# Performance work log

Measured on AMD Instinct MI355X. Metric: run time of the kernel, lower is better.

## Reference

```python
import jax, jax.numpy as jnp
import numpy as np

D_MODEL = 4096
D_FF = 11008

def _dequant_matmul(x, w_int, s):
    # x: [N, in], w_int: [out, in] int, s: [out, 1] -> [N, out]
    w = w_int.astype(jnp.float32) * s  # dequantized weight [out, in]
    return x @ w.T

def setup_inputs() -> dict:
    key = jax.random.key(0)
    ks = jax.random.split(key, 7)
    x = jax.random.normal(ks[0], (4, 2048, D_MODEL), dtype=jnp.float32)
    gate_w = jax.random.randint(ks[1], (D_FF, D_MODEL), -128, 128, dtype=jnp.int32)
    up_w = jax.random.randint(ks[2], (D_FF, D_MODEL), -128, 128, dtype=jnp.int32)
    down_w = jax.random.randint(ks[3], (D_MODEL, D_FF), -128, 128, dtype=jnp.int32)
    gate_s = jax.random.uniform(ks[4], (D_FF, 1), dtype=jnp.float32) * 0.01
    up_s = jax.random.uniform(ks[5], (D_FF, 1), dtype=jnp.float32) * 0.01
    down_s = jax.random.uniform(ks[6], (D_MODEL, 1), dtype=jnp.float32) * 0.01
    return {"x": x, "gate_w": gate_w, "gate_s": gate_s, "up_w": up_w,
            "up_s": up_s, "down_w": down_w, "down_s": down_s}

def reference(x, gate_w, gate_s, up_w, up_s, down_w, down_s):
    batch, seq_len, hidden = x.shape
    x_flat = x.reshape(-1, hidden).astype(jnp.float32)
    gate = _dequant_matmul(x_flat, gate_w, gate_s)
    up = _dequant_matmul(x_flat, up_w, up_s)
    h = jax.nn.silu(gate) * up
    out = _dequant_matmul(h, down_w, down_s)
    return out.astype(x.dtype).reshape(batch, seq_len, hidden)
```

## Files before the change

### kernel.cpp

```cpp
#include <hip/hip_runtime.h>


typedef __attribute__((ext_vector_type(8))) __bf16 bf16x8;
typedef __attribute__((ext_vector_type(4))) float f32x4;
typedef __attribute__((ext_vector_type(8))) unsigned short ushort8;
typedef __attribute__((ext_vector_type(4))) int i32x4;

#define D_MODEL 4096
#define D_FF    11008
#define NTOK    8192

static __device__ __forceinline__ unsigned short f32_to_bf16(float f) {
    union { float f; unsigned u; } v; v.f = f;
    unsigned r = v.u + 0x7fffu + ((v.u >> 16) & 1u);
    return (unsigned short)(r >> 16);
}
static __device__ __forceinline__ void gload_lds16(const void* g, void* l) {
    __builtin_amdgcn_global_load_lds(
        (const __attribute__((address_space(1))) void*)g,
        (__attribute__((address_space(3))) void*)l, 16, 0, 0);
}

__global__ __launch_bounds__(256)
void pack_gu_kernel(const int* __restrict__ gw, const int* __restrict__ uw,
                    signed char* __restrict__ out)
{
    long long i = ((long long)blockIdx.x * 256 + threadIdx.x) * 8;
    const int r = (int)(i >> 12);
    const int k = (int)(i & 4095);
    const int src_row = ((r >> 5) << 4) + (r & 15);
    const int* src = ((r >> 4) & 1) ? uw : gw;
    const int* p = src + (size_t)src_row * D_MODEL + k;
    int4 w0 = *(const int4*)(p);
    int4 w1 = *(const int4*)(p + 4);
    union { signed char c[8]; unsigned long long u; } rr;
    rr.c[0] = (signed char)w0.x; rr.c[1] = (signed char)w0.y;
    rr.c[2] = (signed char)w0.z; rr.c[3] = (signed char)w0.w;
    rr.c[4] = (signed char)w1.x; rr.c[5] = (signed char)w1.y;
    rr.c[6] = (signed char)w1.z; rr.c[7] = (signed char)w1.w;
    *(unsigned long long*)(out + i) = rr.u;
}

__global__ __launch_bounds__(256)
void dequant_w_kernel(const int* __restrict__ w, const float* __restrict__ s,
                      unsigned short* __restrict__ out, int cols, long long total)
{
    long long i = ((long long)blockIdx.x * 256 + threadIdx.x) * 8;
    if (i >= total) return;
    float sc = s[(int)(i / cols)];
    int4 w0 = *(const int4*)(w + i);
    int4 w1 = *(const int4*)(w + i + 4);
    ushort8 r;
    r[0] = f32_to_bf16((float)w0.x * sc);
    r[1] = f32_to_bf16((float)w0.y * sc);
    r[2] = f32_to_bf16((float)w0.z * sc);
    r[3] = f32_to_bf16((float)w0.w * sc);
    r[4] = f32_to_bf16((float)w1.x * sc);
    r[5] = f32_to_bf16((float)w1.y * sc);
    r[6] = f32_to_bf16((float)w1.z * sc);
    r[7] = f32_to_bf16((float)w1.w * sc);
    *(ushort8*)(out + i) = r;
}

__global__ __launch_bounds__(256)
void quant_x_kernel(const float* __restrict__ x, signed char* __restrict__ xq,
                    float* __restrict__ xs)
{
    __shared__ float red[4];
    const int row = blockIdx.x;
    const int t   = threadIdx.x;
    const float* xr = x + (size_t)row * D_MODEL;
    float4 v0 = *(const float4*)(xr + t * 16);
    float4 v1 = *(const float4*)(xr + t * 16 + 4);
    float4 v2 = *(const float4*)(xr + t * 16 + 8);
    float4 v3 = *(const float4*)(xr + t * 16 + 12);
    float m = fabsf(v0.x);
    m = fmaxf(m, fabsf(v0.y)); m = fmaxf(m, fabsf(v0.z)); m = fmaxf(m, fabsf(v0.w));
    m = fmaxf(m, fabsf(v1.x)); m = fmaxf(m, fabsf(v1.y)); m = fmaxf(m, fabsf(v1.z)); m = fmaxf(m, fabsf(v1.w));
    m = fmaxf(m, fabsf(v2.x)); m = fmaxf(m, fabsf(v2.y)); m = fmaxf(m, fabsf(v2.z)); m = fmaxf(m, fabsf(v2.w));
    m = fmaxf(m, fabsf(v3.x)); m = fmaxf(m, fabsf(v3.y)); m = fmaxf(m, fabsf(v3.z)); m = fmaxf(m, fabsf(v3.w));
    #pragma unroll
    for (int o = 32; o > 0; o >>= 1) m = fmaxf(m, __shfl_xor(m, o));
    if ((t & 63) == 0) red[t >> 6] = m;
    __syncthreads();
    m = fmaxf(fmaxf(red[0], red[1]), fmaxf(red[2], red[3]));
    m = fmaxf(m, 1e-20f);
    const float inv = 127.0f / m;
    if (t == 0) xs[row] = m / 127.0f;
    union { signed char c[16]; int4 i; } r;
    #pragma unroll
    for (int j = 0; j < 4; ++j) {
        float4 v = (j == 0) ? v0 : (j == 1) ? v1 : (j == 2) ? v2 : v3;
        r.c[j*4+0] = (signed char)(int)rintf(fminf(fmaxf(v.x*inv,-127.f),127.f));
        r.c[j*4+1] = (signed char)(int)rintf(fminf(fmaxf(v.y*inv,-127.f),127.f));
        r.c[j*4+2] = (signed char)(int)rintf(fminf(fmaxf(v.z*inv,-127.f),127.f));
        r.c[j*4+3] = (signed char)(int)rintf(fminf(fmaxf(v.w*inv,-127.f),127.f));
    }
    *(int4*)(xq + (size_t)row * D_MODEL + t * 16) = r.i;
}

__global__ __launch_bounds__(512, 2)
void gemm_i8gu(const signed char* __restrict__ A,
               const signed char* __restrict__ B,
               unsigned short* __restrict__ H,
               const float* __restrict__ xs,
               const float* __restrict__ gs,
               const float* __restrict__ us,
               int M, int NH, int K)
{
    extern __shared__ char smem[];
    const int tid = threadIdx.x;
    const int l   = tid & 63;
    const int w   = tid >> 6;
    const int wm  = w >> 2;
    const int wn  = w & 3;

    const int nbx  = gridDim.x;
    const int nwg  = nbx * gridDim.y;
    const int orig = blockIdx.y * nbx + blockIdx.x;
    const int cpx  = nwg >> 3;
    const int swz  = (orig & 7) * cpx + (orig >> 3);
    const int bn = swz % nbx, bm = swz / nbx;
    const int m0 = bm * 256, n0 = bn * 256;

    const int st_r = tid >> 2;
    const int st_c = ((tid & 3) ^ ((st_r >> 1) & 3)) << 4;
    const signed char* gA = A + (size_t)(m0 + st_r) * K + st_c;
    const signed char* gB = B + (size_t)(n0 + st_r) * K + st_c;
    const size_t ld128 = (size_t)128 * K;

    const int s4v = l >> 4;
    const int rA = wm * 128 + (l & 15);
    const int rB = wn * 64  + (l & 15);
    const int offA = rA * 64 + ((s4v << 4) ^ (((rA >> 1) & 3) << 4));
    const int offB = 16384 + rB * 64 + ((s4v << 4) ^ (((rB >> 1) & 3) << 4));

    i32x4 acc[8][4] = {};
    i32x4 af[8], bfr[4];

#define SBAR()  __builtin_amdgcn_sched_barrier(0)
#define BAR()   __builtin_amdgcn_s_barrier()
#define VM4()   asm volatile("s_waitcnt vmcnt(4)" ::: "memory")

#define ST_A8(SS, NXT) do { \
    const signed char* p_ = gA + ((size_t)(SS) << 6); \
    gload_lds16(p_,         smem + (NXT) + (w << 10)); \
    gload_lds16(p_ + ld128, smem + (NXT) + 8192 + (w << 10)); } while (0)
#define ST_B8(SS, NXT) do { \
    const signed char* p_ = gB + ((size_t)(SS) << 6); \
    gload_lds16(p_,         smem + (NXT) + 16384 + (w << 10)); \
    gload_lds16(p_ + 16384 - 8192 + 0, smem, 0); } while (0)
#undef ST_B8
#define ST_B8(SS, NXT) do { \
    const signed char* p_ = gB + ((size_t)(SS) << 6); \
    gload_lds16(p_,         smem + (NXT) + 16384 + (w << 10)); \
    gload_lds16(p_ + ld128, smem + (NXT) + 16384 + 8192 + (w << 10)); } while (0)

#define STEP8(CUR, NXT, SS) do { \
    ST_A8(SS, NXT); \
    ST_B8(SS, NXT); \
    af[0] = *(const i32x4*)(smem + (CUR) + offA); \
    af[1] = *(const i32x4*)(smem + (CUR) + offA + 1024); \
    af[2] = *(const i32x4*)(smem + (CUR) + offA + 2048); \
    af[3] = *(const i32x4*)(smem + (CUR) + offA + 3072); \
    af[4] = *(const i32x4*)(smem + (CUR) + offA + 4096); \
    af[5] = *(const i32x4*)(smem + (CUR) + offA + 5120); \
    af[6] = *(const i32x4*)(smem + (CUR) + offA + 6144); \
    af[7] = *(const i32x4*)(smem + (CUR) + offA + 7168); \
    bfr[0] = *(const i32x4*)(smem + (CUR) + offB); \
    bfr[1] = *(const i32x4*)(smem + (CUR) + offB + 1024); \
    bfr[2] = *(const i32x4*)(smem + (CUR) + offB + 2048); \
    bfr[3] = *(const i32x4*)(smem + (CUR) + offB + 3072); \
    __builtin_amdgcn_s_setprio(1); \
    _Pragma("unroll") \
    for (int mi_ = 0; mi_ < 8; ++mi_) { \
        _Pragma("unroll") \
        for (int ni_ = 0; ni_ < 4; ++ni_) { \
            acc[mi_][ni_] = __builtin_amdgcn_mfma_i32_16x16x64_i8( \
                af[mi_], bfr[ni_], acc[mi_][ni_], 0, 0, 0); \
        } } \
    __builtin_amdgcn_s_setprio(0); \
    VM4(); SBAR(); BAR(); \
} while (0)

    ST_A8(0, 0);      ST_B8(0, 0);
    ST_A8(1, 32768);  ST_B8(1, 32768);
    VM4(); SBAR(); BAR();

    const int T = K >> 6;
    #pragma unroll 1
    for (int s = 0; s < T; s += 4) {
        int s2 = s + 2; if (s2 >= T) s2 -= T;
        int s3 = s + 3; if (s3 >= T) s3 -= T;
        int s4 = s + 4; if (s4 >= T) s4 -= T;
        int s5 = s + 5; if (s5 >= T) s5 -= T;
        STEP8(0,     65536, s2);
        STEP8(32768, 98304, s3);
        STEP8(65536, 0,     s4);
        STEP8(98304, 32768, s5);
    }
    asm volatile("s_waitcnt vmcnt(0)" ::: "memory");

    const int er = (l >> 4) * 4;
    const int ec = l & 15;
    const int hbase = (n0 >> 1) + wn * 32;
    #pragma unroll
    for (int mi = 0; mi < 8; ++mi) {
        const int rowb = m0 + wm * 128 + mi * 16 + er;
        const float4 xsv = *(const float4*)(xs + rowb);
        #pragma unroll
        for (int p = 0; p < 2; ++p) {
            const int c = hbase + p * 16 + ec;
            const float sg = gs[c];
            const float su = us[c];
            #pragma unroll
            for (int q = 0; q < 4; ++q) {
                const float xsc = (q == 0) ? xsv.x : (q == 1) ? xsv.y
                                 : (q == 2) ? xsv.z : xsv.w;
                float g = (float)acc[mi][2*p][q]     * sg * xsc;
                float u = (float)acc[mi][2*p + 1][q] * su * xsc;
                float sig = 1.0f / (1.0f + __expf(-g));
                H[(size_t)(rowb + q) * NH + c] = f32_to_bf16(g * sig * u);
            }
        }
    }
#undef STEP8
#undef ST_A8
#undef ST_B8
#undef VM4
#undef BAR
#undef SBAR
}

__global__ __launch_bounds__(512, 2)
void gemm256_down(const unsigned short* __restrict__ A,
                  const unsigned short* __restrict__ B,
                  float* __restrict__ C,
                  int M, int N, int K)
{
    extern __shared__ char smem[];
    const int tid = threadIdx.x;
    const int l   = tid & 63;
    const int w   = tid >> 6;
    const int wm  = w >> 2;
    const int wn  = w & 3;

    const int nbx  = gridDim.x;
    const int nwg  = nbx * gridDim.y;
    const int orig = blockIdx.y * nbx + blockIdx.x;
    const int cpx  = nwg >> 3;
    const int swz  = (orig & 7) * cpx + (orig >> 3);
    const int bn = swz % nbx, bm = swz / nbx;
    const int m0 = bm * 256, n0 = bn * 256;

    const int st_r = tid >> 2;
    const int st_c = ((tid & 3) ^ ((st_r >> 1) & 3)) << 3;
    const unsigned short* gA = A + (size_t)(m0 + st_r) * K + st_c;
    const unsigned short* gB = B + (size_t)(n0 + st_r) * K + st_c;
    const size_t ld128 = (size_t)128 * K;

    const int s4v = l >> 4;
    const int rA = wm * 128 + (l & 15);
    const int rB = wn * 64  + (l & 15);
    const int offA = rA * 64 + ((s4v << 4) ^ (((rA >> 1) & 3) << 4));
    const int offB = 16384 + rB * 64 + ((s4v << 4) ^ (((rB >> 1) & 3) << 4));

    f32x4 acc[8][4] = {};
    bf16x8 af[8], bfr[4];

#define SBAR()  __builtin_amdgcn_sched_barrier(0)
#define BAR()   __builtin_amdgcn_s_barrier()
#define VM4()   asm volatile("s_waitcnt vmcnt(4)" ::: "memory")

#define ST_A2(SS, NXT) do { \
    const unsigned short* p_ = gA + ((size_t)(SS) << 5); \
    gload_lds16(p_,         smem + (NXT) + (w << 10)); \
    gload_lds16(p_ + ld128, smem + (NXT) + 8192 + (w << 10)); } while (0)
#define ST_B2(SS, NXT) do { \
    const unsigned short* p_ = gB + ((size_t)(SS) << 5); \
    gload_lds16(p_,         smem + (NXT) + 16384 + (w << 10)); \
    gload_lds16(p_ + ld128, smem + (NXT) + 16384 + 8192 + (w << 10)); } while (0)

#define STEPD(CUR, NXT, SS) do { \
    ST_A2(SS, NXT); \
    ST_B2(SS, NXT); \
    af[0] = *(const bf16x8*)(smem + (CUR) + offA); \
    af[1] = *(const bf16x8*)(smem + (CUR) + offA + 1024); \
    af[2] = *(const bf16x8*)(smem + (CUR) + offA + 2048); \
    af[3] = *(const bf16x8*)(smem + (CUR) + offA + 3072); \
    af[4] = *(const bf16x8*)(smem + (CUR) + offA + 4096); \
    af[5] = *(const bf16x8*)(smem + (CUR) + offA + 5120); \
    af[6] = *(const bf16x8*)(smem + (CUR) + offA + 6144); \
    af[7] = *(const bf16x8*)(smem + (CUR) + offA + 7168); \
    bfr[0] = *(const bf16x8*)(smem + (CUR) + offB); \
    bfr[1] = *(const bf16x8*)(smem + (CUR) + offB + 1024); \
    bfr[2] = *(const bf16x8*)(smem + (CUR) + offB + 2048); \
    bfr[3] = *(const bf16x8*)(smem + (CUR) + offB + 3072); \
    __builtin_amdgcn_s_setprio(1); \
    _Pragma("unroll") \
    for (int mi_ = 0; mi_ < 8; ++mi_) { \
        _Pragma("unroll") \
        for (int ni_ = 0; ni_ < 4; ++ni_) { \
            acc[mi_][ni_] = __builtin_amdgcn_mfma_f32_16x16x32_bf16( \
                af[mi_], bfr[ni_], acc[mi_][ni_], 0, 0, 0); \
        } } \
    __builtin_amdgcn_s_setprio(0); \
    VM4(); SBAR(); BAR(); \
} while (0)

    ST_A2(0, 0);      ST_B2(0, 0);
    ST_A2(1, 32768);  ST_B2(1, 32768);
    VM4(); SBAR(); BAR();

    const int T = K >> 5;
    #pragma unroll 1
    for (int s = 0; s < T; s += 4) {
        int s2 = s + 2; if (s2 >= T) s2 -= T;
        int s3 = s + 3; if (s3 >= T) s3 -= T;
        int s4 = s + 4; if (s4 >= T) s4 -= T;
        int s5 = s + 5; if (s5 >= T) s5 -= T;
        STEPD(0,     65536, s2);
        STEPD(32768, 98304, s3);
        STEPD(65536, 0,     s4);
        STEPD(98304, 32768, s5);
    }
    asm volatile("s_waitcnt vmcnt(0)" ::: "memory");

    const int er = (l >> 4) * 4;
    const int ec = l & 15;
    #pragma unroll
    for (int mi = 0; mi < 8; ++mi) {
        #pragma unroll
        for (int ni = 0; ni < 4; ++ni) {
            #pragma unroll
            for (int q = 0; q < 4; ++q) {
                int row = m0 + wm * 128 + mi * 16 + er + q;
                int col = n0 + wn * 64  + ni * 16 + ec;
                C[(size_t)row * N + col] = acc[mi][ni][q];
            }
        }
    }
#undef STEPD
#undef ST_A2
#undef ST_B2
#undef VM4
#undef BAR
#undef SBAR
}

extern "C" void kernel_launch(void* const* d_in, const int* in_sizes, int n_in,
                              void* d_out, int out_size, void* d_ws, size_t ws_size,
                              hipStream_t stream)
{
    const float* x  = (const float*)d_in[0];
    const int*   gw = (const int*)  d_in[1];
    const float* gs = (const float*)d_in[2];
    const int*   uw = (const int*)  d_in[3];
    const float* us = (const float*)d_in[4];
    const int*   dw = (const int*)  d_in[5];
    const float* dsc= (const float*)d_in[6];

    char* ws = (char*)d_ws;
    signed char*    Xq   = (signed char*)ws;    ws += (size_t)NTOK * D_MODEL;
    float*          xs   = (float*)ws;          ws += (size_t)NTOK * 4;
    signed char*    Wgu8 = (signed char*)ws;    ws += (size_t)2 * D_FF * D_MODEL;
    unsigned short* Wd   = (unsigned short*)ws; ws += (size_t)D_MODEL * D_FF * 2;
    unsigned short* H    = (unsigned short*)ws;

    const long long wtot  = (long long)D_FF * D_MODEL;
    const long long gutot = 2LL * wtot;

    hipFuncSetAttribute(reinterpret_cast<const void*>(gemm_i8gu),
                        hipFuncAttributeMaxDynamicSharedMemorySize, 131072);
    hipFuncSetAttribute(reinterpret_cast<const void*>(gemm256_down),
                        hipFuncAttributeMaxDynamicSharedMemorySize, 131072);

    pack_gu_kernel  <<<(int)(gutot / 2048), 256, 0, stream>>>(gw, uw, Wgu8);
    dequant_w_kernel<<<(int)(wtot  / 2048), 256, 0, stream>>>(dw, dsc, Wd, D_FF, wtot);
    quant_x_kernel  <<<NTOK, 256, 0, stream>>>(x, Xq, xs);

    dim3 g1(2 * D_FF / 256, NTOK / 256);
    gemm_i8gu<<<g1, 512, 131072, stream>>>(Xq, Wgu8, H, xs, gs, us,
                                           NTOK, D_FF, D_MODEL);

    dim3 g3(D_MODEL / 256, NTOK / 256);
    gemm256_down<<<g3, 512, 131072, stream>>>(H, Wd, (float*)d_out,
                                              NTOK, D_MODEL, D_FF);
}
```

Measured before the change: 1.555 ms.

## Deepen LDS prefetch to three stages and double-buffer B fragments in registers

Both GEMM kernels now issue global-to-LDS loads three K-steps ahead instead of two across the four-buffer LDS ring. They also load the next step's B fragments into a second register set while the current step's MFMAs run on the first. The aim is to hide more global-memory and LDS-read latency behind the matrix instructions. In exchange, each thread holds more live VGPRs, which risks pressure or spills under the 512-thread, 2-block launch bounds. The unchanged vmcnt(4) wait now forces two stages to land before each barrier, which may limit how much extra overlap is actually gained.

Result: no change. 1.563 ms (+0.5%).

```diff
diff --git a/kernel.cpp b/kernel.cpp
--- a/kernel.cpp
+++ b/kernel.cpp
@@ -136,7 +136,8 @@
     const int offB = 16384 + rB * 64 + ((s4v << 4) ^ (((rB >> 1) & 3) << 4));
 
     i32x4 acc[8][4] = {};
-    i32x4 af[8], bfr[4];
+    i32x4 af[8];
+    i32x4 bfa[4], bfb[4];
 
 #define SBAR()  __builtin_amdgcn_sched_barrier(0)
 #define BAR()   __builtin_amdgcn_s_barrier()
@@ -149,14 +150,15 @@
 #define ST_B8(SS, NXT) do { \
     const signed char* p_ = gB + ((size_t)(SS) << 6); \
     gload_lds16(p_,         smem + (NXT) + 16384 + (w << 10)); \
-    gload_lds16(p_ + 16384 - 8192 + 0, smem, 0); } while (0)
-#undef ST_B8
-#define ST_B8(SS, NXT) do { \
-    const signed char* p_ = gB + ((size_t)(SS) << 6); \
-    gload_lds16(p_,         smem + (NXT) + 16384 + (w << 10)); \
     gload_lds16(p_ + ld128, smem + (NXT) + 16384 + 8192 + (w << 10)); } while (0)
 
-#define STEP8(CUR, NXT, SS) do { \
+#define LD_BFR(BQ, BASE) do { \
+    BQ[0] = *(const i32x4*)(smem + (BASE) + offB); \
+    BQ[1] = *(const i32x4*)(smem + (BASE) + offB + 1024); \
+    BQ[2] = *(const i32x4*)(smem + (BASE) + offB + 2048); \
+    BQ[3] = *(const i32x4*)(smem + (BASE) + offB + 3072); } while (0)
+
+#define STEP8(CUR, RD, NXT, SS, BC, BN) do { \
     ST_A8(SS, NXT); \
     ST_B8(SS, NXT); \
     af[0] = *(const i32x4*)(smem + (CUR) + offA); \
@@ -167,17 +169,14 @@
     af[5] = *(const i32x4*)(smem + (CUR) + offA + 5120); \
     af[6] = *(const i32x4*)(smem + (CUR) + offA + 6144); \
     af[7] = *(const i32x4*)(smem + (CUR) + offA + 7168); \
-    bfr[0] = *(const i32x4*)(smem + (CUR) + offB); \
-    bfr[1] = *(const i32x4*)(smem + (CUR) + offB + 1024); \
-    bfr[2] = *(const i32x4*)(smem + (CUR) + offB + 2048); \
-    bfr[3] = *(const i32x4*)(smem + (CUR) + offB + 3072); \
+    LD_BFR(BN, RD); \
     __builtin_amdgcn_s_setprio(1); \
     _Pragma("unroll") \
     for (int mi_ = 0; mi_ < 8; ++mi_) { \
         _Pragma("unroll") \
         for (int ni_ = 0; ni_ < 4; ++ni_) { \
             acc[mi_][ni_] = __builtin_amdgcn_mfma_i32_16x16x64_i8( \
-                af[mi_], bfr[ni_], acc[mi_][ni_], 0, 0, 0); \
+                af[mi_], BC[ni_], acc[mi_][ni_], 0, 0, 0); \
         } } \
     __builtin_amdgcn_s_setprio(0); \
     VM4(); SBAR(); BAR(); \
@@ -185,19 +184,22 @@
 
     ST_A8(0, 0);      ST_B8(0, 0);
     ST_A8(1, 32768);  ST_B8(1, 32768);
-    VM4(); SBAR(); BAR();
+    ST_A8(2, 65536);  ST_B8(2, 65536);
+    VM4();
+    LD_BFR(bfa, 0);
+    SBAR(); BAR();
 
     const int T = K >> 6;
     #pragma unroll 1
     for (int s = 0; s < T; s += 4) {
-        int s2 = s + 2; if (s2 >= T) s2 -= T;
         int s3 = s + 3; if (s3 >= T) s3 -= T;
         int s4 = s + 4; if (s4 >= T) s4 -= T;
         int s5 = s + 5; if (s5 >= T) s5 -= T;
-        STEP8(0,     65536, s2);
-        STEP8(32768, 98304, s3);
-        STEP8(65536, 0,     s4);
-        STEP8(98304, 32768, s5);
+        int s6 = s + 6; if (s6 >= T) s6 -= T;
+        STEP8(0,     32768, 98304, s3, bfa, bfb);
+        STEP8(32768, 65536, 0,     s4, bfb, bfa);
+        STEP8(65536, 98304, 32768, s5, bfa, bfb);
+        STEP8(98304, 0,     65536, s6, bfb, bfa);
     }
     asm volatile("s_waitcnt vmcnt(0)" ::: "memory");
 
@@ -225,6 +227,7 @@
         }
     }
 #undef STEP8
+#undef LD_BFR
 #undef ST_A8
 #undef ST_B8
 #undef VM4
@@ -266,7 +269,8 @@
     const int offB = 16384 + rB * 64 + ((s4v << 4) ^ (((rB >> 1) & 3) << 4));
 
     f32x4 acc[8][4] = {};
-    bf16x8 af[8], bfr[4];
+    bf16x8 af[8];
+    bf16x8 bfa[4], bfb[4];
 
 #define SBAR()  __builtin_amdgcn_sched_barrier(0)
 #define BAR()   __builtin_amdgcn_s_barrier()
@@ -281,7 +285,13 @@
     gload_lds16(p_,         smem + (NXT) + 16384 + (w << 10)); \
     gload_lds16(p_ + ld128, smem + (NXT) + 16384 + 8192 + (w << 10)); } while (0)
 
-#define STEPD(CUR, NXT, SS) do { \
+#define LD_BFRD(BQ, BASE) do { \
+    BQ[0] = *(const bf16x8*)(smem + (BASE) + offB); \
+    BQ[1] = *(const bf16x8*)(smem + (BASE) + offB + 1024); \
+    BQ[2] = *(const bf16x8*)(smem + (BASE) + offB + 2048); \
+    BQ[3] = *(const bf16x8*)(smem + (BASE) + offB + 3072); } while (0)
+
+#define STEPD(CUR, RD, NXT, SS, BC, BN) do { \
     ST_A2(SS, NXT); \
     ST_B2(SS, NXT); \
     af[0] = *(const bf16x8*)(smem + (CUR) + offA); \
@@ -292,17 +302,14 @@
     af[5] = *(const bf16x8*)(smem + (CUR) + offA + 5120); \
     af[6] = *(const bf16x8*)(smem + (CUR) + offA + 6144); \
     af[7] = *(const bf16x8*)(smem + (CUR) + offA + 7168); \
-    bfr[0] = *(const bf16x8*)(smem + (CUR) + offB); \
-    bfr[1] = *(const bf16x8*)(smem + (CUR) + offB + 1024); \
-    bfr[2] = *(const bf16x8*)(smem + (CUR) + offB + 2048); \
-    bfr[3] = *(const bf16x8*)(smem + (CUR) + offB + 3072); \
+    LD_BFRD(BN, RD); \
     __builtin_amdgcn_s_setprio(1); \
     _Pragma("unroll") \
     for (int mi_ = 0; mi_ < 8; ++mi_) { \
         _Pragma("unroll") \
         for (int ni_ = 0; ni_ < 4; ++ni_) { \
             acc[mi_][ni_] = __builtin_amdgcn_mfma_f32_16x16x32_bf16( \
-                af[mi_], bfr[ni_], acc[mi_][ni_], 0, 0, 0); \
+                af[mi_], BC[ni_], acc[mi_][ni_], 0, 0, 0); \
         } } \
     __builtin_amdgcn_s_setprio(0); \
     VM4(); SBAR(); BAR(); \
@@ -310,19 +317,22 @@
 
     ST_A2(0, 0);      ST_B2(0, 0);
     ST_A2(1, 32768);  ST_B2(1, 32768);
-    VM4(); SBAR(); BAR();
+    ST_A2(2, 65536);  ST_B2(2, 65536);
+    VM4();
+    LD_BFRD(bfa, 0);
+    SBAR(); BAR();
 
     const int T = K >> 5;
     #pragma unroll 1
     for (int s = 0; s < T; s += 4) {
-        int s2 = s + 2; if (s2 >= T) s2 -= T;
         int s3 = s + 3; if (s3 >= T) s3 -= T;
         int s4 = s + 4; if (s4 >= T) s4 -= T;
         int s5 = s + 5; if (s5 >= T) s5 -= T;
-        STEPD(0,     65536, s2);
-        STEPD(32768, 98304, s3);
-        STEPD(65536, 0,     s4);
-        STEPD(98304, 32768, s5);
+        int s6 = s + 6; if (s6 >= T) s6 -= T;
+        STEPD(0,     32768, 98304, s3, bfa, bfb);
+        STEPD(32768, 65536, 0,     s4, bfb, bfa);
+        STEPD(65536, 98304, 32768, s5, bfa, bfb);
+        STEPD(98304, 0,     65536, s6, bfb, bfa);
     }
     asm volatile("s_waitcnt vmcnt(0)" ::: "memory");
 
@@ -341,6 +351,7 @@
         }
     }
 #undef STEPD
+#undef LD_BFRD
 #undef ST_A2
 #undef ST_B2
 #undef VM4
```

## Shrink GEMM tiles to 256x128 with 4 waves and triple-buffered LDS

Applied to the files above, without the earlier changes.

Both GEMM kernels move from a 256x256 tile with 8 waves and a 4-stage LDS ring (128KB) to a 256x128 tile with 4 waves and a 3-stage ring (72KB). Per-wave accumulator work is unchanged, but each block now loads more A rows per wave. The smaller LDS footprint allows two blocks per CU, which is meant to improve overlap and tail balance across the larger grid. In exchange, the lower B reuse per block raises global and L2 traffic for A, since each A tile is now loaded twice as often.

After: 1.730 ms. 11.3% more time.

```diff
diff --git a/kernel.cpp b/kernel.cpp
--- a/kernel.cpp
+++ b/kernel.cpp
@@ -99,7 +99,7 @@
     *(int4*)(xq + (size_t)row * D_MODEL + t * 16) = r.i;
 }
 
-__global__ __launch_bounds__(512, 2)
+__global__ __launch_bounds__(256, 2)
 void gemm_i8gu(const signed char* __restrict__ A,
                const signed char* __restrict__ B,
                unsigned short* __restrict__ H,
@@ -112,8 +112,8 @@
     const int tid = threadIdx.x;
     const int l   = tid & 63;
     const int w   = tid >> 6;
-    const int wm  = w >> 2;
-    const int wn  = w & 3;
+    const int wm  = w >> 1;
+    const int wn  = w & 1;
 
     const int nbx  = gridDim.x;
     const int nwg  = nbx * gridDim.y;
@@ -121,13 +121,13 @@
     const int cpx  = nwg >> 3;
     const int swz  = (orig & 7) * cpx + (orig >> 3);
     const int bn = swz % nbx, bm = swz / nbx;
-    const int m0 = bm * 256, n0 = bn * 256;
-
-    const int st_r = tid >> 2;
-    const int st_c = ((tid & 3) ^ ((st_r >> 1) & 3)) << 4;
-    const signed char* gA = A + (size_t)(m0 + st_r) * K + st_c;
-    const signed char* gB = B + (size_t)(n0 + st_r) * K + st_c;
-    const size_t ld128 = (size_t)128 * K;
+    const int m0 = bm * 256, n0 = bn * 128;
+
+    const int sr0 = w * 16 + (l >> 2);
+    const int sc  = ((l & 3) ^ ((sr0 >> 1) & 3)) << 4;
+    const signed char* gA = A + (size_t)(m0 + sr0) * K + sc;
+    const signed char* gB = B + (size_t)(n0 + sr0) * K + sc;
+    const size_t ld64 = (size_t)64 * K;
 
     const int s4v = l >> 4;
     const int rA = wm * 128 + (l & 15);
@@ -138,27 +138,26 @@
     i32x4 acc[8][4] = {};
     i32x4 af[8], bfr[4];
 
+    const int BUF = 24576;
+
 #define SBAR()  __builtin_amdgcn_sched_barrier(0)
 #define BAR()   __builtin_amdgcn_s_barrier()
-#define VM4()   asm volatile("s_waitcnt vmcnt(4)" ::: "memory")
-
-#define ST_A8(SS, NXT) do { \
+#define VM6()   asm volatile("s_waitcnt vmcnt(6)" ::: "memory")
+
+#define ST_A(SS, NXT) do { \
     const signed char* p_ = gA + ((size_t)(SS) << 6); \
-    gload_lds16(p_,         smem + (NXT) + (w << 10)); \
-    gload_lds16(p_ + ld128, smem + (NXT) + 8192 + (w << 10)); } while (0)
-#define ST_B8(SS, NXT) do { \
+    gload_lds16(p_,            smem + (NXT) +         (w << 10)); \
+    gload_lds16(p_ + ld64,     smem + (NXT) + 4096  + (w << 10)); \
+    gload_lds16(p_ + 2 * ld64, smem + (NXT) + 8192  + (w << 10)); \
+    gload_lds16(p_ + 3 * ld64, smem + (NXT) + 12288 + (w << 10)); } while (0)
+#define ST_B(SS, NXT) do { \
     const signed char* p_ = gB + ((size_t)(SS) << 6); \
-    gload_lds16(p_,         smem + (NXT) + 16384 + (w << 10)); \
-    gload_lds16(p_ + 16384 - 8192 + 0, smem, 0); } while (0)
-#undef ST_B8
-#define ST_B8(SS, NXT) do { \
-    const signed char* p_ = gB + ((size_t)(SS) << 6); \
-    gload_lds16(p_,         smem + (NXT) + 16384 + (w << 10)); \
-    gload_lds16(p_ + ld128, smem + (NXT) + 16384 + 8192 + (w << 10)); } while (0)
+    gload_lds16(p_,        smem + (NXT) + 16384 + (w << 10)); \
+    gload_lds16(p_ + ld64, smem + (NXT) + 20480 + (w << 10)); } while (0)
 
 #define STEP8(CUR, NXT, SS) do { \
-    ST_A8(SS, NXT); \
-    ST_B8(SS, NXT); \
+    ST_A(SS, NXT); \
+    ST_B(SS, NXT); \
     af[0] = *(const i32x4*)(smem + (CUR) + offA); \
     af[1] = *(const i32x4*)(smem + (CUR) + offA + 1024); \
     af[2] = *(const i32x4*)(smem + (CUR) + offA + 2048); \
@@ -180,24 +179,21 @@
                 af[mi_], bfr[ni_], acc[mi_][ni_], 0, 0, 0); \
         } } \
     __builtin_amdgcn_s_setprio(0); \
-    VM4(); SBAR(); BAR(); \
+    VM6(); SBAR(); BAR(); \
 } while (0)
 
-    ST_A8(0, 0);      ST_B8(0, 0);
-    ST_A8(1, 32768);  ST_B8(1, 32768);
-    VM4(); SBAR(); BAR();
+    ST_A(0, 0);    ST_B(0, 0);
+    ST_A(1, BUF);  ST_B(1, BUF);
+    VM6(); SBAR(); BAR();
 
     const int T = K >> 6;
+    int cur = 0, nxt = 2 * BUF;
     #pragma unroll 1
-    for (int s = 0; s < T; s += 4) {
-        int s2 = s + 2; if (s2 >= T) s2 -= T;
-        int s3 = s + 3; if (s3 >= T) s3 -= T;
-        int s4 = s + 4; if (s4 >= T) s4 -= T;
-        int s5 = s + 5; if (s5 >= T) s5 -= T;
-        STEP8(0,     65536, s2);
-        STEP8(32768, 98304, s3);
-        STEP8(65536, 0,     s4);
-        STEP8(98304, 32768, s5);
+    for (int s = 0; s < T; ++s) {
+        int ss = s + 2; if (ss >= T) ss -= T;
+        STEP8(cur, nxt, ss);
+        cur += BUF; if (cur == 3 * BUF) cur = 0;
+        nxt += BUF; if (nxt == 3 * BUF) nxt = 0;
     }
     asm volatile("s_waitcnt vmcnt(0)" ::: "memory");
 
@@ -225,14 +221,14 @@
         }
     }
 #undef STEP8
-#undef ST_A8
-#undef ST_B8
-#undef VM4
+#undef ST_A
+#undef ST_B
+#undef VM6
 #undef BAR
 #undef SBAR
 }
 
-__global__ __launch_bounds__(512, 2)
+__global__ __launch_bounds__(256, 2)
 void gemm256_down(const unsigned short* __restrict__ A,
                   const unsigned short* __restrict__ B,
                   float* __restrict__ C,
@@ -242,8 +238,8 @@
     const int tid = threadIdx.x;
     const int l   = tid & 63;
     const int w   = tid >> 6;
-    const int wm  = w >> 2;
-    const int wn  = w & 3;
+    const int wm  = w >> 1;
+    const int wn  = w & 1;
 
     const int nbx  = gridDim.x;
     const int nwg  = nbx * gridDim.y;
@@ -251,13 +247,13 @@
     const int cpx  = nwg >> 3;
     const int swz  = (orig & 7) * cpx + (orig >> 3);
     const int bn = swz % nbx, bm = swz / nbx;
-    const int m0 = bm * 256, n0 = bn * 256;
-
-    const int st_r = tid >> 2;
-    const int st_c = ((tid & 3) ^ ((st_r >> 1) & 3)) << 3;
-    const unsigned short* gA = A + (size_t)(m0 + st_r) * K + st_c;
-    const unsigned short* gB = B + (size_t)(n0 + st_r) * K + st_c;
-    const size_t ld128 = (size_t)128 * K;
+    const int m0 = bm * 256, n0 = bn * 128;
+
+    const int sr0 = w * 16 + (l >> 2);
+    const int sc  = ((l & 3) ^ ((sr0 >> 1) & 3)) << 3;
+    const unsigned short* gA = A + (size_t)(m0 + sr0) * K + sc;
+    const unsigned short* gB = B + (size_t)(n0 + sr0) * K + sc;
+    const size_t ld64 = (size_t)64 * K;
 
     const int s4v = l >> 4;
     const int rA = wm * 128 + (l & 15);
@@ -268,18 +264,22 @@
     f32x4 acc[8][4] = {};
     bf16x8 af[8], bfr[4];
 
+    const int BUF = 24576;
+
 #define SBAR()  __builtin_amdgcn_sched_barrier(0)
 #define BAR()   __builtin_amdgcn_s_barrier()
-#define VM4()   asm volatile("s_waitcnt vmcnt(4)" ::: "memory")
+#define VM6()   asm volatile("s_waitcnt vmcnt(6)" ::: "memory")
 
 #define ST_A2(SS, NXT) do { \
     const unsigned short* p_ = gA + ((size_t)(SS) << 5); \
-    gload_lds16(p_,         smem + (NXT) + (w << 10)); \
-    gload_lds16(p_ + ld128, smem + (NXT) + 8192 + (w << 10)); } while (0)
+    gload_lds16(p_,            smem + (NXT) +         (w << 10)); \
+    gload_lds16(p_ + ld64,     smem + (NXT) + 4096  + (w << 10)); \
+    gload_lds16(p_ + 2 * ld64, smem + (NXT) + 8192  + (w << 10)); \
+    gload_lds16(p_ + 3 * ld64, smem + (NXT) + 12288 + (w << 10)); } while (0)
 #define ST_B2(SS, NXT) do { \
     const unsigned short* p_ = gB + ((size_t)(SS) << 5); \
-    gload_lds16(p_,         smem + (NXT) + 16384 + (w << 10)); \
-    gload_lds16(p_ + ld128, smem + (NXT) + 16384 + 8192 + (w << 10)); } while (0)
+    gload_lds16(p_,        smem + (NXT) + 16384 + (w << 10)); \
+    gload_lds16(p_ + ld64, smem + (NXT) + 20480 + (w << 10)); } while (0)
 
 #define STEPD(CUR, NXT, SS) do { \
     ST_A2(SS, NXT); \
@@ -305,24 +305,21 @@
                 af[mi_], bfr[ni_], acc[mi_][ni_], 0, 0, 0); \
         } } \
     __builtin_amdgcn_s_setprio(0); \
-    VM4(); SBAR(); BAR(); \
+    VM6(); SBAR(); BAR(); \
 } while (0)
 
-    ST_A2(0, 0);      ST_B2(0, 0);
-    ST_A2(1, 32768);  ST_B2(1, 32768);
-    VM4(); SBAR(); BAR();
+    ST_A2(0, 0);    ST_B2(0, 0);
+    ST_A2(1, BUF);  ST_B2(1, BUF);
+    VM6(); SBAR(); BAR();
 
     const int T = K >> 5;
+    int cur = 0, nxt = 2 * BUF;
     #pragma unroll 1
-    for (int s = 0; s < T; s += 4) {
-        int s2 = s + 2; if (s2 >= T) s2 -= T;
-        int s3 = s + 3; if (s3 >= T) s3 -= T;
-        int s4 = s + 4; if (s4 >= T) s4 -= T;
-        int s5 = s + 5; if (s5 >= T) s5 -= T;
-        STEPD(0,     65536, s2);
-        STEPD(32768, 98304, s3);
-        STEPD(65536, 0,     s4);
-        STEPD(98304, 32768, s5);
+    for (int s = 0; s < T; ++s) {
+        int ss = s + 2; if (ss >= T) ss -= T;
+        STEPD(cur, nxt, ss);
+        cur += BUF; if (cur == 3 * BUF) cur = 0;
+        nxt += BUF; if (nxt == 3 * BUF) nxt = 0;
     }
     asm volatile("s_waitcnt vmcnt(0)" ::: "memory");
 
@@ -343,7 +340,7 @@
 #undef STEPD
 #undef ST_A2
 #undef ST_B2
-#undef VM4
+#undef VM6
 #undef BAR
 #undef SBAR
 }
@@ -371,19 +368,19 @@
     const long long gutot = 2LL * wtot;
 
     hipFuncSetAttribute(reinterpret_cast<const void*>(gemm_i8gu),
-                        hipFuncAttributeMaxDynamicSharedMemorySize, 131072);
+                        hipFuncAttributeMaxDynamicSharedMemorySize, 73728);
     hipFuncSetAttribute(reinterpret_cast<const void*>(gemm256_down),
-                        hipFuncAttributeMaxDynamicSharedMemorySize, 131072);
+                        hipFuncAttributeMaxDynamicSharedMemorySize, 73728);
 
     pack_gu_kernel  <<<(int)(gutot / 2048), 256, 0, stream>>>(gw, uw, Wgu8);
     dequant_w_kernel<<<(int)(wtot  / 2048), 256, 0, stream>>>(dw, dsc, Wd, D_FF, wtot);
     quant_x_kernel  <<<NTOK, 256, 0, stream>>>(x, Xq, xs);
 
-    dim3 g1(2 * D_FF / 256, NTOK / 256);
-    gemm_i8gu<<<g1, 512, 131072, stream>>>(Xq, Wgu8, H, xs, gs, us,
-                                           NTOK, D_FF, D_MODEL);
-
-    dim3 g3(D_MODEL / 256, NTOK / 256);
-    gemm256_down<<<g3, 512, 131072, stream>>>(H, Wd, (float*)d_out,
-                                              NTOK, D_MODEL, D_FF);
-}
+    dim3 g1(2 * D_FF / 128, NTOK / 256);
+    gemm_i8gu<<<g1, 256, 73728, stream>>>(Xq, Wgu8, H, xs, gs, us,
+                                          NTOK, D_FF, D_MODEL);
+
+    dim3 g3(D_MODEL / 128, NTOK / 256);
+    gemm256_down<<<g3, 256, 73728, stream>>>(H, Wd, (float*)d_out,
+                                             NTOK, D_MODEL, D_FF);
+}
```

## Use 4-wave 256x256 GEMM tiles with register double-buffered fragments and deeper prefetch

Applied to the files above, without the earlier changes.

Both GEMM kernels move from 8 waves per block to 4 waves, each wave now computing a 128x128 sub-tile (8x8 MFMA accumulators). LDS fragments for the next k-step are loaded into a second register set while the current step's MFMAs run, and the global-to-LDS prefetch distance grows from 2 to 3 stages. The aim is to raise MFMA-to-LDS-read intensity and hide LDS and global latency better. In exchange, register pressure rises sharply (64 accumulators plus four fragment arrays) with fewer waves per CU to hide stalls, so spills or lower occupancy are possible.

Measured after the change: 1.633 ms. +5.0%, slower.

```diff
diff --git a/kernel.cpp b/kernel.cpp
--- a/kernel.cpp
+++ b/kernel.cpp
@@ -99,7 +99,7 @@
     *(int4*)(xq + (size_t)row * D_MODEL + t * 16) = r.i;
 }
 
-__global__ __launch_bounds__(512, 2)
+__global__ __launch_bounds__(256, 1)
 void gemm_i8gu(const signed char* __restrict__ A,
                const signed char* __restrict__ B,
                unsigned short* __restrict__ H,
@@ -112,8 +112,8 @@
     const int tid = threadIdx.x;
     const int l   = tid & 63;
     const int w   = tid >> 6;
-    const int wm  = w >> 2;
-    const int wn  = w & 3;
+    const int wm  = w >> 1;
+    const int wn  = w & 1;
 
     const int nbx  = gridDim.x;
     const int nwg  = nbx * gridDim.y;
@@ -123,93 +123,93 @@
     const int bn = swz % nbx, bm = swz / nbx;
     const int m0 = bm * 256, n0 = bn * 256;
 
-    const int st_r = tid >> 2;
-    const int st_c = ((tid & 3) ^ ((st_r >> 1) & 3)) << 4;
+    const int st_r = w * 64 + (l >> 2);
+    const int st_c = ((l & 3) ^ ((st_r >> 1) & 3)) << 4;
     const signed char* gA = A + (size_t)(m0 + st_r) * K + st_c;
     const signed char* gB = B + (size_t)(n0 + st_r) * K + st_c;
-    const size_t ld128 = (size_t)128 * K;
+    const size_t ld16 = (size_t)16 * K;
 
     const int s4v = l >> 4;
     const int rA = wm * 128 + (l & 15);
-    const int rB = wn * 64  + (l & 15);
+    const int rB = wn * 128 + (l & 15);
     const int offA = rA * 64 + ((s4v << 4) ^ (((rA >> 1) & 3) << 4));
     const int offB = 16384 + rB * 64 + ((s4v << 4) ^ (((rB >> 1) & 3) << 4));
 
-    i32x4 acc[8][4] = {};
-    i32x4 af[8], bfr[4];
+    i32x4 acc[8][8] = {};
+    i32x4 a0[8], b0[8], a1[8], b1[8];
 
 #define SBAR()  __builtin_amdgcn_sched_barrier(0)
 #define BAR()   __builtin_amdgcn_s_barrier()
-#define VM4()   asm volatile("s_waitcnt vmcnt(4)" ::: "memory")
-
-#define ST_A8(SS, NXT) do { \
-    const signed char* p_ = gA + ((size_t)(SS) << 6); \
-    gload_lds16(p_,         smem + (NXT) + (w << 10)); \
-    gload_lds16(p_ + ld128, smem + (NXT) + 8192 + (w << 10)); } while (0)
-#define ST_B8(SS, NXT) do { \
-    const signed char* p_ = gB + ((size_t)(SS) << 6); \
-    gload_lds16(p_,         smem + (NXT) + 16384 + (w << 10)); \
-    gload_lds16(p_ + 16384 - 8192 + 0, smem, 0); } while (0)
-#undef ST_B8
-#define ST_B8(SS, NXT) do { \
-    const signed char* p_ = gB + ((size_t)(SS) << 6); \
-    gload_lds16(p_,         smem + (NXT) + 16384 + (w << 10)); \
-    gload_lds16(p_ + ld128, smem + (NXT) + 16384 + 8192 + (w << 10)); } while (0)
-
-#define STEP8(CUR, NXT, SS) do { \
-    ST_A8(SS, NXT); \
-    ST_B8(SS, NXT); \
-    af[0] = *(const i32x4*)(smem + (CUR) + offA); \
-    af[1] = *(const i32x4*)(smem + (CUR) + offA + 1024); \
-    af[2] = *(const i32x4*)(smem + (CUR) + offA + 2048); \
-    af[3] = *(const i32x4*)(smem + (CUR) + offA + 3072); \
-    af[4] = *(const i32x4*)(smem + (CUR) + offA + 4096); \
-    af[5] = *(const i32x4*)(smem + (CUR) + offA + 5120); \
-    af[6] = *(const i32x4*)(smem + (CUR) + offA + 6144); \
-    af[7] = *(const i32x4*)(smem + (CUR) + offA + 7168); \
-    bfr[0] = *(const i32x4*)(smem + (CUR) + offB); \
-    bfr[1] = *(const i32x4*)(smem + (CUR) + offB + 1024); \
-    bfr[2] = *(const i32x4*)(smem + (CUR) + offB + 2048); \
-    bfr[3] = *(const i32x4*)(smem + (CUR) + offB + 3072); \
+#define VM8()   asm volatile("s_waitcnt vmcnt(8)" ::: "memory")
+
+#define ST_AB(SS, SLOT) do { \
+    const signed char* pa_ = gA + ((size_t)(SS) << 6); \
+    const signed char* pb_ = gB + ((size_t)(SS) << 6); \
+    gload_lds16(pa_,            smem + (SLOT) + (w << 12)); \
+    gload_lds16(pa_ + ld16,     smem + (SLOT) + (w << 12) + 1024); \
+    gload_lds16(pa_ + 2 * ld16, smem + (SLOT) + (w << 12) + 2048); \
+    gload_lds16(pa_ + 3 * ld16, smem + (SLOT) + (w << 12) + 3072); \
+    gload_lds16(pb_,            smem + (SLOT) + 16384 + (w << 12)); \
+    gload_lds16(pb_ + ld16,     smem + (SLOT) + 16384 + (w << 12) + 1024); \
+    gload_lds16(pb_ + 2 * ld16, smem + (SLOT) + 16384 + (w << 12) + 2048); \
+    gload_lds16(pb_ + 3 * ld16, smem + (SLOT) + 16384 + (w << 12) + 3072); } while (0)
+
+#define LD_FRAGS(FA, FB, SLOT) do { \
+    _Pragma("unroll") \
+    for (int f_ = 0; f_ < 8; ++f_) { \
+        FA[f_] = *(const i32x4*)(smem + (SLOT) + offA + (f_ << 10)); \
+        FB[f_] = *(const i32x4*)(smem + (SLOT) + offB + (f_ << 10)); \
+    } } while (0)
+
+#define MFMA64(FA, FB) do { \
     __builtin_amdgcn_s_setprio(1); \
     _Pragma("unroll") \
     for (int mi_ = 0; mi_ < 8; ++mi_) { \
         _Pragma("unroll") \
-        for (int ni_ = 0; ni_ < 4; ++ni_) { \
+        for (int ni_ = 0; ni_ < 8; ++ni_) { \
             acc[mi_][ni_] = __builtin_amdgcn_mfma_i32_16x16x64_i8( \
-                af[mi_], bfr[ni_], acc[mi_][ni_], 0, 0, 0); \
+                FA[mi_], FB[ni_], acc[mi_][ni_], 0, 0, 0); \
         } } \
-    __builtin_amdgcn_s_setprio(0); \
-    VM4(); SBAR(); BAR(); \
+    __builtin_amdgcn_s_setprio(0); } while (0)
+
+#define STEP(PRE, NXT, SS, CA, CB, NA, NB) do { \
+    ST_AB(SS, NXT); \
+    LD_FRAGS(NA, NB, PRE); \
+    SBAR(); \
+    MFMA64(CA, CB); \
+    SBAR(); \
+    VM8(); BAR(); \
 } while (0)
 
-    ST_A8(0, 0);      ST_B8(0, 0);
-    ST_A8(1, 32768);  ST_B8(1, 32768);
-    VM4(); SBAR(); BAR();
+    ST_AB(0, 0);
+    ST_AB(1, 32768);
+    ST_AB(2, 65536);
+    VM8(); SBAR(); BAR();
+    LD_FRAGS(a0, b0, 0);
 
     const int T = K >> 6;
     #pragma unroll 1
     for (int s = 0; s < T; s += 4) {
-        int s2 = s + 2; if (s2 >= T) s2 -= T;
         int s3 = s + 3; if (s3 >= T) s3 -= T;
         int s4 = s + 4; if (s4 >= T) s4 -= T;
         int s5 = s + 5; if (s5 >= T) s5 -= T;
-        STEP8(0,     65536, s2);
-        STEP8(32768, 98304, s3);
-        STEP8(65536, 0,     s4);
-        STEP8(98304, 32768, s5);
+        int s6 = s + 6; if (s6 >= T) s6 -= T;
+        STEP(32768, 98304, s3, a0, b0, a1, b1);
+        STEP(65536, 0,     s4, a1, b1, a0, b0);
+        STEP(98304, 32768, s5, a0, b0, a1, b1);
+        STEP(0,     65536, s6, a1, b1, a0, b0);
     }
     asm volatile("s_waitcnt vmcnt(0)" ::: "memory");
 
     const int er = (l >> 4) * 4;
     const int ec = l & 15;
-    const int hbase = (n0 >> 1) + wn * 32;
+    const int hbase = (n0 >> 1) + wn * 64;
     #pragma unroll
     for (int mi = 0; mi < 8; ++mi) {
         const int rowb = m0 + wm * 128 + mi * 16 + er;
         const float4 xsv = *(const float4*)(xs + rowb);
         #pragma unroll
-        for (int p = 0; p < 2; ++p) {
+        for (int p = 0; p < 4; ++p) {
             const int c = hbase + p * 16 + ec;
             const float sg = gs[c];
             const float su = us[c];
@@ -224,15 +224,16 @@
             }
         }
     }
-#undef STEP8
-#undef ST_A8
-#undef ST_B8
-#undef VM4
+#undef STEP
+#undef MFMA64
+#undef LD_FRAGS
+#undef ST_AB
+#undef VM8
 #undef BAR
 #undef SBAR
 }
 
-__global__ __launch_bounds__(512, 2)
+__global__ __launch_bounds__(256, 1)
 void gemm256_down(const unsigned short* __restrict__ A,
                   const unsigned short* __restrict__ B,
                   float* __restrict__ C,
@@ -242,8 +243,8 @@
     const int tid = threadIdx.x;
     const int l   = tid & 63;
     const int w   = tid >> 6;
-    const int wm  = w >> 2;
-    const int wn  = w & 3;
+    const int wm  = w >> 1;
+    const int wn  = w & 1;
 
     const int nbx  = gridDim.x;
     const int nwg  = nbx * gridDim.y;
@@ -253,76 +254,81 @@
     const int bn = swz % nbx, bm = swz / nbx;
     const int m0 = bm * 256, n0 = bn * 256;
 
-    const int st_r = tid >> 2;
-    const int st_c = ((tid & 3) ^ ((st_r >> 1) & 3)) << 3;
+    const int st_r = w * 64 + (l >> 2);
+    const int st_c = ((l & 3) ^ ((st_r >> 1) & 3)) << 3;
     const unsigned short* gA = A + (size_t)(m0 + st_r) * K + st_c;
     const unsigned short* gB = B + (size_t)(n0 + st_r) * K + st_c;
-    const size_t ld128 = (size_t)128 * K;
+    const size_t ld16 = (size_t)16 * K;
 
     const int s4v = l >> 4;
     const int rA = wm * 128 + (l & 15);
-    const int rB = wn * 64  + (l & 15);
+    const int rB = wn * 128 + (l & 15);
     const int offA = rA * 64 + ((s4v << 4) ^ (((rA >> 1) & 3) << 4));
     const int offB = 16384 + rB * 64 + ((s4v << 4) ^ (((rB >> 1) & 3) << 4));
 
-    f32x4 acc[8][4] = {};
-    bf16x8 af[8], bfr[4];
+    f32x4 acc[8][8] = {};
+    bf16x8 a0[8], b0[8], a1[8], b1[8];
 
 #define SBAR()  __builtin_amdgcn_sched_barrier(0)
 #define BAR()   __builtin_amdgcn_s_barrier()
-#define VM4()   asm volatile("s_waitcnt vmcnt(4)" ::: "memory")
-
-#define ST_A2(SS, NXT) do { \
-    const unsigned short* p_ = gA + ((size_t)(SS) << 5); \
-    gload_lds16(p_,         smem + (NXT) + (w << 10)); \
-    gload_lds16(p_ + ld128, smem + (NXT) + 8192 + (w << 10)); } while (0)
-#define ST_B2(SS, NXT) do { \
-    const unsigned short* p_ = gB + ((size_t)(SS) << 5); \
-    gload_lds16(p_,         smem + (NXT) + 16384 + (w << 10)); \
-    gload_lds16(p_ + ld128, smem + (NXT) + 16384 + 8192 + (w << 10)); } while (0)
-
-#define STEPD(CUR, NXT, SS) do { \
-    ST_A2(SS, NXT); \
-    ST_B2(SS, NXT); \
-    af[0] = *(const bf16x8*)(smem + (CUR) + offA); \
-    af[1] = *(const bf16x8*)(smem + (CUR) + offA + 1024); \
-    af[2] = *(const bf16x8*)(smem + (CUR) + offA + 2048); \
-    af[3] = *(const bf16x8*)(smem + (CUR) + offA + 3072); \
-    af[4] = *(const bf16x8*)(smem + (CUR) + offA + 4096); \
-    af[5] = *(const bf16x8*)(smem + (CUR) + offA + 5120); \
-    af[6] = *(const bf16x8*)(smem + (CUR) + offA + 6144); \
-    af[7] = *(const bf16x8*)(smem + (CUR) + offA + 7168); \
-    bfr[0] = *(const bf16x8*)(smem + (CUR) + offB); \
-    bfr[1] = *(const bf16x8*)(smem + (CUR) + offB + 1024); \
-    bfr[2] = *(const bf16x8*)(smem + (CUR) + offB + 2048); \
-    bfr[3] = *(const bf16x8*)(smem + (CUR) + offB + 3072); \
+#define VM8()   asm volatile("s_waitcnt vmcnt(8)" ::: "memory")
+
+#define ST_AB(SS, SLOT) do { \
+    const unsigned short* pa_ = gA + ((size_t)(SS) << 5); \
+    const unsigned short* pb_ = gB + ((size_t)(SS) << 5); \
+    gload_lds16(pa_,            smem + (SLOT) + (w << 12)); \
+    gload_lds16(pa_ + ld16,     smem + (SLOT) + (w << 12) + 1024); \
+    gload_lds16(pa_ + 2 * ld16, smem + (SLOT) + (w << 12) + 2048); \
+    gload_lds16(pa_ + 3 * ld16, smem + (SLOT) + (w << 12) + 3072); \
+    gload_lds16(pb_,            smem + (SLOT) + 16384 + (w << 12)); \
+    gload_lds16(pb_ + ld16,     smem + (SLOT) + 16384 + (w << 12) + 1024); \
+    gload_lds16(pb_ + 2 * ld16, smem + (SLOT) + 16384 + (w << 12) + 2048); \
+    gload_lds16(pb_ + 3 * ld16, smem + (SLOT) + 16384 + (w << 12) + 3072); } while (0)
+
+#define LD_FRAGS(FA, FB, SLOT) do { \
+    _Pragma("unroll") \
+    for (int f_ = 0; f_ < 8; ++f_) { \
+        FA[f_] = *(const bf16x8*)(smem + (SLOT) + offA + (f_ << 10)); \
+        FB[f_] = *(const bf16x8*)(smem + (SLOT) + offB + (f_ << 10)); \
+    } } while (0)
+
+#define MFMA64(FA, FB) do { \
     __builtin_amdgcn_s_setprio(1); \
     _Pragma("unroll") \
     for (int mi_ = 0; mi_ < 8; ++mi_) { \
         _Pragma("unroll") \
-        for (int ni_ = 0; ni_ < 4; ++ni_) { \
+        for (int ni_ = 0; ni_ < 8; ++ni_) { \
             acc[mi_][ni_] = __builtin_amdgcn_mfma_f32_16x16x32_bf16( \
-                af[mi_], bfr[ni_], acc[mi_][ni_], 0, 0, 0); \
+                FA[mi_], FB[ni_], acc[mi_][ni_], 0, 0, 0); \
         } } \
-    __builtin_amdgcn_s_setprio(0); \
-    VM4(); SBAR(); BAR(); \
+    __builtin_amdgcn_s_setprio(0); } while (0)
+
+#define STEP(PRE, NXT, SS, CA, CB, NA, NB) do { \
+    ST_AB(SS, NXT); \
+    LD_FRAGS(NA, NB, PRE); \
+    SBAR(); \
+    MFMA64(CA, CB); \
+    SBAR(); \
+    VM8(); BAR(); \
 } while (0)
 
-    ST_A2(0, 0);      ST_B2(0, 0);
-    ST_A2(1, 32768);  ST_B2(1, 32768);
-    VM4(); SBAR(); BAR();
+    ST_AB(0, 0);
+    ST_AB(1, 32768);
+    ST_AB(2, 65536);
+    VM8(); SBAR(); BAR();
+    LD_FRAGS(a0, b0, 0);
 
     const int T = K >> 5;
     #pragma unroll 1
     for (int s = 0; s < T; s += 4) {
-        int s2 = s + 2; if (s2 >= T) s2 -= T;
         int s3 = s + 3; if (s3 >= T) s3 -= T;
         int s4 = s + 4; if (s4 >= T) s4 -= T;
         int s5 = s + 5; if (s5 >= T) s5 -= T;
-        STEPD(0,     65536, s2);
-        STEPD(32768, 98304, s3);
-        STEPD(65536, 0,     s4);
-        STEPD(98304, 32768, s5);
+        int s6 = s + 6; if (s6 >= T) s6 -= T;
+        STEP(32768, 98304, s3, a0, b0, a1, b1);
+        STEP(65536, 0,     s4, a1, b1, a0, b0);
+        STEP(98304, 32768, s5, a0, b0, a1, b1);
+        STEP(0,     65536, s6, a1, b1, a0, b0);
     }
     asm volatile("s_waitcnt vmcnt(0)" ::: "memory");
 
@@ -331,19 +337,20 @@
     #pragma unroll
     for (int mi = 0; mi < 8; ++mi) {
         #pragma unroll
-        for (int ni = 0; ni < 4; ++ni) {
+        for (int ni = 0; ni < 8; ++ni) {
             #pragma unroll
             for (int q = 0; q < 4; ++q) {
                 int row = m0 + wm * 128 + mi * 16 + er + q;
-                int col = n0 + wn * 64  + ni * 16 + ec;
+                int col = n0 + wn * 128 + ni * 16 + ec;
                 C[(size_t)row * N + col] = acc[mi][ni][q];
             }
         }
     }
-#undef STEPD
-#undef ST_A2
-#undef ST_B2
-#undef VM4
+#undef STEP
+#undef MFMA64
+#undef LD_FRAGS
+#undef ST_AB
+#undef VM8
 #undef BAR
 #undef SBAR
 }
@@ -380,10 +387,10 @@
     quant_x_kernel  <<<NTOK, 256, 0, stream>>>(x, Xq, xs);
 
     dim3 g1(2 * D_FF / 256, NTOK / 256);
-    gemm_i8gu<<<g1, 512, 131072, stream>>>(Xq, Wgu8, H, xs, gs, us,
+    gemm_i8gu<<<g1, 256, 131072, stream>>>(Xq, Wgu8, H, xs, gs, us,
                                            NTOK, D_FF, D_MODEL);
 
     dim3 g3(D_MODEL / 256, NTOK / 256);
-    gemm256_down<<<g3, 512, 131072, stream>>>(H, Wd, (float*)d_out,
+    gemm256_down<<<g3, 256, 131072, stream>>>(H, Wd, (float*)d_out,
                                               NTOK, D_MODEL, D_FF);
 }
```
